# Kernel tuning notes

Hardware: AMD Instinct MI355X
Metric: run time of the kernel (lower is better)

The kernel has to match this reference:

```python
import jax, jax.numpy as jnp
import numpy as np

N_NODES = 50000
N_EDGES = 800000
F_NODE = 64
F_EDGE = 32
F_GLOBAL = 32
OUT_DIM = 64
N_GRAPHS = 256


def setup_inputs() -> dict:
    key = jax.random.key(0)
    ks = jax.random.split(key, 8)
    x = jax.random.normal(ks[0], (N_NODES, F_NODE), dtype=jnp.float32)
    edge_index = jax.random.randint(ks[1], (2, N_EDGES), 0, N_NODES, dtype=jnp.int64)
    edge_attr = jax.random.normal(ks[2], (N_EDGES, F_EDGE), dtype=jnp.float32)
    u = jax.random.normal(ks[3], (N_GRAPHS, F_GLOBAL), dtype=jnp.float32)
    batch = jnp.sort(jax.random.randint(ks[4], (N_NODES,), 0, N_GRAPHS, dtype=jnp.int64))
    # params (scaled like default Linear init)
    W1 = jax.random.normal(ks[5], (F_NODE + F_EDGE, OUT_DIM), dtype=jnp.float32) / np.sqrt(F_NODE + F_EDGE)
    b1 = jnp.zeros((OUT_DIM,), dtype=jnp.float32)
    W2 = jax.random.normal(ks[6], (F_NODE + OUT_DIM + F_GLOBAL, OUT_DIM), dtype=jnp.float32) / np.sqrt(F_NODE + OUT_DIM + F_GLOBAL)
    b2 = jnp.zeros((OUT_DIM,), dtype=jnp.float32)
    return {"x": x, "edge_index": edge_index, "edge_attr": edge_attr,
            "u": u, "batch": batch, "W1": W1, "b1": b1, "W2": W2, "b2": b2}


def reference(x, edge_index, edge_attr, u, batch, W1, b1, W2, b2):
    dest, src = edge_index[0], edge_index[1]
    # gather source node features + edge attrs -> [E, F_NODE + F_EDGE]
    edge_info = jnp.concatenate([x[src], edge_attr], axis=1)
    # node_mlp_1: Linear + ReLU
    edge_messages = jax.nn.relu(edge_info @ W1 + b1)  # [E, OUT_DIM]
    # scatter-sum into destination nodes
    aggregated = jax.ops.segment_sum(edge_messages, dest, num_segments=x.shape[0])  # [N, OUT_DIM]
    # concat node, aggregated messages, per-graph global
    node_info = jnp.concatenate([x, aggregated, u[batch]], axis=1)  # [N, F_NODE+OUT_DIM+F_GLOBAL]
    # node_mlp_2: Linear + ReLU
    return jax.nn.relu(node_info @ W2 + b2)  # [N, OUT_DIM]
```

## Files before the change

### kernel.cpp

```cpp
#include <hip/hip_runtime.h>
#include <hip/hip_bf16.h>

typedef __attribute__((ext_vector_type(8))) short short8;
typedef __attribute__((ext_vector_type(4))) float f32x4;

constexpr int NN = 50000;
constexpr int NE = 800000;
constexpr int FN = 64;
constexpr int FE = 32;
constexpr int FG = 32;
constexpr int OD = 64;
constexpr int NG = 256;

constexpr int SCAN_B = 256;
constexpr int NBLK = (NN + SCAN_B - 1) / SCAN_B;

constexpr int SLOTS_MAX = NE + 15 * NN;
constexpr int AGG_BLOCKS = 2048;
constexpr int AGG_WAVES  = AGG_BLOCKS * 4;
constexpr int NWIN       = NN / 16;
constexpr int NODE_BLOCKS = 512;
constexpr int NODE_WAVES  = NODE_BLOCKS * 4;

static __device__ __forceinline__ unsigned pack_bf16(float a, float b) {
    __hip_bfloat162 h = __float22bfloat162_rn(float2{a, b});
    return *reinterpret_cast<unsigned*>(&h);
}
static __device__ __forceinline__ float bf16r(float v) {
    __hip_bfloat16 h = __float2bfloat16(v);
    return __bfloat162float(h);
}

__global__ __launch_bounds__(256) void k_fill(int2* __restrict__ bucket,
                                              int* __restrict__ cnt,
                                              unsigned* __restrict__ xb32) {
    const int i = blockIdx.x * 256 + threadIdx.x;
    if (i < SLOTS_MAX) bucket[i] = make_int2(NN, 0);
    if (i < NN) cnt[i] = 0;
    if (i < 32) xb32[NN * 32 + i] = 0;
}

__global__ __launch_bounds__(256) void k_xcvt(const float* __restrict__ x,
                                              unsigned* __restrict__ xb32) {
    const int i = blockIdx.x * 256 + threadIdx.x;
    if (i >= NN * FN / 8) return;
    const float4* p = (const float4*)(x + (size_t)i * 8);
    float4 f0 = p[0], f1 = p[1];
    uint4 o;
    o.x = pack_bf16(f0.x, f0.y);
    o.y = pack_bf16(f0.z, f0.w);
    o.z = pack_bf16(f1.x, f1.y);
    o.w = pack_bf16(f1.z, f1.w);
    ((uint4*)xb32)[i] = o;
}

__global__ __launch_bounds__(256) void k_pre(const float* __restrict__ u,
                                             const float* __restrict__ W2,
                                             const float* __restrict__ b2,
                                             const float* __restrict__ ea,
                                             const float* __restrict__ W1,
                                             const float* __restrict__ b1,
                                             float* __restrict__ uW2b,
                                             float* __restrict__ corr) {
    if (blockIdx.x == NG / 4) {
        const int j = threadIdx.x;
        if (j < OD) {
            float acc = b1[j];
#pragma unroll
            for (int k = 0; k < FE; ++k) {
                const float ek = bf16r(ea[k]);
                const float wk = bf16r(W1[(FN + k) * OD + j]);
                acc = fmaf(ek, wk, acc);
            }
            corr[j] = fmaxf(acc, 0.0f);
        }
        return;
    }
    const int lane = threadIdx.x & 63;
    float wcol[FG];
#pragma unroll
    for (int k = 0; k < FG; ++k) wcol[k] = W2[(FN + OD + k) * OD + lane];
    const float bias = b2[lane];

    int g = (blockIdx.x * blockDim.x + threadIdx.x) >> 6;
    g = __builtin_amdgcn_readfirstlane(g);
    if (g >= NG) return;

    const float* __restrict__ urow = u + (size_t)g * FG;
    float acc = bias;
#pragma unroll
    for (int k = 0; k < FG; ++k) acc = fmaf(urow[k], wcol[k], acc);
    uW2b[(size_t)g * OD + lane] = acc;
}

__global__ __launch_bounds__(256) void k_hist(const int* __restrict__ ei,
                                              int* __restrict__ cnt) {
    const int e = blockIdx.x * blockDim.x + threadIdx.x;
    if (e < NE) atomicAdd(&cnt[ei[e]], 1);
}

__global__ __launch_bounds__(SCAN_B) void k_scan1(const int* __restrict__ cnt,
                                                  int* __restrict__ pstart,
                                                  int* __restrict__ bsum) {
    __shared__ int lds[SCAN_B];
    const int i = blockIdx.x * SCAN_B + threadIdx.x;
    const int v = (i < NN) ? (((cnt[i] + 15) >> 4) << 4) : 0;
    lds[threadIdx.x] = v;
    __syncthreads();
#pragma unroll
    for (int off = 1; off < SCAN_B; off <<= 1) {
        int t = (threadIdx.x >= off) ? lds[threadIdx.x - off] : 0;
        __syncthreads();
        lds[threadIdx.x] += t;
        __syncthreads();
    }
    const int incl = lds[threadIdx.x];
    if (i < NN) pstart[i] = incl - v;
    if (threadIdx.x == SCAN_B - 1) bsum[blockIdx.x] = incl;
}

__global__ __launch_bounds__(SCAN_B) void k_scan2(const int* __restrict__ bsum,
                                                  int* __restrict__ bscan) {
    __shared__ int lds[SCAN_B];
    const int i = threadIdx.x;
    const int v = (i < NBLK) ? bsum[i] : 0;
    lds[i] = v;
    __syncthreads();
#pragma unroll
    for (int off = 1; off < SCAN_B; off <<= 1) {
        int t = (i >= off) ? lds[i - off] : 0;
        __syncthreads();
        lds[i] += t;
        __syncthreads();
    }
    if (i < NBLK) bscan[i] = lds[i] - v;
}

__global__ __launch_bounds__(SCAN_B) void k_scan3(int* __restrict__ pstart,
                                                  const int* __restrict__ bscan,
                                                  const int* __restrict__ cnt,
                                                  int* __restrict__ cursor) {
    const int i = blockIdx.x * SCAN_B + threadIdx.x;
    if (i < NN) {
        const int s = pstart[i] + bscan[blockIdx.x];
        pstart[i] = s;
        cursor[i] = s;
        if (i == NN - 1) pstart[NN] = s + (((cnt[i] + 15) >> 4) << 4);
    }
}

__global__ __launch_bounds__(256) void k_scatter(const int* __restrict__ ei,
                                                 int* __restrict__ cursor,
                                                 int2* __restrict__ bucket) {
    const int e = blockIdx.x * blockDim.x + threadIdx.x;
    if (e < NE) {
        const int dst = ei[e];
        const int src = ei[NE + e];
        const int pos = atomicAdd(&cursor[dst], 1);
        bucket[pos] = make_int2(src, e);
    }
}

__global__ __launch_bounds__(256) void k_aggw(const int2* __restrict__ bucket,
                                              const float* __restrict__ ea,
                                              const unsigned short* __restrict__ xb,
                                              const float* __restrict__ W1,
                                              const float* __restrict__ b1,
                                              const int* __restrict__ pstart,
                                              float* __restrict__ partial) {
    const int l = threadIdx.x & 63;
    const int g = l >> 4;
    const int c = l & 15;

    short8 wf[3][4];
#pragma unroll
    for (int t = 0; t < 3; ++t)
#pragma unroll
        for (int b = 0; b < 4; ++b)
#pragma unroll
            for (int i = 0; i < 8; i += 2) {
                const int k = 32 * t + 8 * g + i;
                const unsigned p = pack_bf16(W1[k * OD + (c + 16 * b)],
                                             W1[(k + 1) * OD + (c + 16 * b)]);
                ((unsigned*)&wf[t][b])[i / 2] = p;
            }
    float bias[4];
#pragma unroll
    for (int b = 0; b < 4; ++b) bias[b] = b1[c + 16 * b];

    const int nwin = pstart[NN] >> 4;

    int wv = (blockIdx.x * blockDim.x + threadIdx.x) >> 6;
    wv = __builtin_amdgcn_readfirstlane(wv);

#pragma unroll 2
    for (int w = wv; w < nwin; w += AGG_WAVES) {
        const int2 se = bucket[(size_t)w * 16 + c];

        short8 a0, a1, a2;
        {
            const uint4* xr = (const uint4*)(xb + (size_t)se.x * FN);
            uint4 q0 = xr[g];
            uint4 q1 = xr[4 + g];
            a0 = *(short8*)&q0;
            a1 = *(short8*)&q1;
        }
        {
            const float4* er = (const float4*)(ea + (size_t)se.y * FE);
            float4 e0 = er[2 * g], e1 = er[2 * g + 1];
            uint4 q2;
            q2.x = pack_bf16(e0.x, e0.y);
            q2.y = pack_bf16(e0.z, e0.w);
            q2.z = pack_bf16(e1.x, e1.y);
            q2.w = pack_bf16(e1.z, e1.w);
            a2 = *(short8*)&q2;
        }

        float sv[4];
#pragma unroll
        for (int b = 0; b < 4; ++b) {
            f32x4 acc = {0.f, 0.f, 0.f, 0.f};
            acc = __builtin_amdgcn_mfma_f32_16x16x32_bf16(a0, wf[0][b], acc, 0, 0, 0);
            acc = __builtin_amdgcn_mfma_f32_16x16x32_bf16(a1, wf[1][b], acc, 0, 0, 0);
            acc = __builtin_amdgcn_mfma_f32_16x16x32_bf16(a2, wf[2][b], acc, 0, 0, 0);
            float s = fmaxf(acc[0] + bias[b], 0.0f) + fmaxf(acc[1] + bias[b], 0.0f)
                    + fmaxf(acc[2] + bias[b], 0.0f) + fmaxf(acc[3] + bias[b], 0.0f);
            s += __shfl_xor(s, 16);
            s += __shfl_xor(s, 32);
            sv[b] = s;
        }
        float v = sv[0];
        v = (g == 1) ? sv[1] : v;
        v = (g == 2) ? sv[2] : v;
        v = (g == 3) ? sv[3] : v;
        partial[(size_t)w * 64 + l] = v;
    }
}

__global__ __launch_bounds__(256) void k_red(const float* __restrict__ partial,
                                             const int* __restrict__ pstart,
                                             const int* __restrict__ cnt,
                                             const float* __restrict__ corr,
                                             unsigned short* __restrict__ aggb) {
    const int l = threadIdx.x & 63;
    int n = (blockIdx.x * blockDim.x + threadIdx.x) >> 6;
    n = __builtin_amdgcn_readfirstlane(n);
    if (n >= NN) return;

    const int w0 = pstart[n] >> 4;
    const int w1 = pstart[n + 1] >> 4;
    float s = 0.0f;
    for (int w = w0; w < w1; ++w) s += partial[(size_t)w * 64 + l];
    const int pads = ((w1 - w0) << 4) - cnt[n];
    s -= (float)pads * corr[l];
    __hip_bfloat16 hb = __float2bfloat16(s);
    aggb[(size_t)n * OD + l] = *reinterpret_cast<unsigned short*>(&hb);
}

__global__ __launch_bounds__(256) void k_nodem(const unsigned short* __restrict__ xb,
                                               const unsigned short* __restrict__ aggb,
                                               const int* __restrict__ bat,
                                               const float* __restrict__ uW2b,
                                               const float* __restrict__ W2,
                                               float* __restrict__ out) {
    const int l = threadIdx.x & 63;
    const int g = l >> 4;
    const int c = l & 15;

    short8 wf[4][4];
#pragma unroll
    for (int t = 0; t < 4; ++t)
#pragma unroll
        for (int b = 0; b < 4; ++b)
#pragma unroll
            for (int i = 0; i < 8; i += 2) {
                const int k = 32 * t + 8 * g + i;
                const unsigned p = pack_bf16(W2[k * OD + (c + 16 * b)],
                                             W2[(k + 1) * OD + (c + 16 * b)]);
                ((unsigned*)&wf[t][b])[i / 2] = p;
            }

    int wv = (blockIdx.x * blockDim.x + threadIdx.x) >> 6;
    wv = __builtin_amdgcn_readfirstlane(wv);

    for (int w = wv; w < NWIN; w += NODE_WAVES) {
        const int n0 = w * 16;
        const uint4* xr = (const uint4*)(xb + (size_t)(n0 + c) * FN);
        const uint4* ar = (const uint4*)(aggb + (size_t)(n0 + c) * OD);
        uint4 qx0 = xr[g], qx1 = xr[4 + g];
        uint4 qa0 = ar[g], qa1 = ar[4 + g];
        short8 a0 = *(short8*)&qx0, a1 = *(short8*)&qx1;
        short8 a2 = *(short8*)&qa0, a3 = *(short8*)&qa1;

        int bq[4];
#pragma unroll
        for (int q = 0; q < 4; ++q) bq[q] = bat[n0 + g * 4 + q];

#pragma unroll
        for (int b = 0; b < 4; ++b) {
            f32x4 acc = {0.f, 0.f, 0.f, 0.f};
            acc = __builtin_amdgcn_mfma_f32_16x16x32_bf16(a0, wf[0][b], acc, 0, 0, 0);
            acc = __builtin_amdgcn_mfma_f32_16x16x32_bf16(a1, wf[1][b], acc, 0, 0, 0);
            acc = __builtin_amdgcn_mfma_f32_16x16x32_bf16(a2, wf[2][b], acc, 0, 0, 0);
            acc = __builtin_amdgcn_mfma_f32_16x16x32_bf16(a3, wf[3][b], acc, 0, 0, 0);
#pragma unroll
            for (int q = 0; q < 4; ++q) {
                const int n = n0 + g * 4 + q;
                const float val = acc[q] + uW2b[(size_t)bq[q] * OD + c + 16 * b];
                out[(size_t)n * OD + c + 16 * b] = fmaxf(val, 0.0f);
            }
        }
    }
}

extern "C" void kernel_launch(void* const* d_in, const int* in_sizes, int n_in,
                              void* d_out, int out_size, void* d_ws, size_t ws_size,
                              hipStream_t stream) {
    const float* x    = (const float*)d_in[0];
    const int*   ei   = (const int*)d_in[1];
    const float* ea   = (const float*)d_in[2];
    const float* u    = (const float*)d_in[3];
    const int*   bat  = (const int*)d_in[4];
    const float* W1   = (const float*)d_in[5];
    const float* b1   = (const float*)d_in[6];
    const float* W2   = (const float*)d_in[7];
    const float* b2   = (const float*)d_in[8];
    float* out = (float*)d_out;

    char* ws = (char*)d_ws;
    auto alloc = [&](size_t bytes) {
        char* p = ws;
        ws += (bytes + 255) & ~size_t(255);
        return p;
    };
    unsigned short* xb   = (unsigned short*)alloc((size_t)(NN + 1) * FN * 2);
    unsigned short* aggb = (unsigned short*)alloc((size_t)NN * OD * 2);
    float* uW2b    = (float*)alloc((size_t)NG * OD * sizeof(float));
    float* corr    = (float*)alloc((size_t)OD * sizeof(float));
    int*   cnt     = (int*)alloc((size_t)NN * sizeof(int));
    int*   pstart  = (int*)alloc((size_t)(NN + 1) * sizeof(int));
    int*   cursor  = (int*)alloc((size_t)NN * sizeof(int));
    int*   bsum    = (int*)alloc((size_t)NBLK * sizeof(int));
    int*   bscan   = (int*)alloc((size_t)NBLK * sizeof(int));
    int2*  bucket  = (int2*)alloc((size_t)SLOTS_MAX * sizeof(int2));
    float* partial = (float*)alloc((size_t)(SLOTS_MAX / 16) * OD * sizeof(float));

    k_fill<<<dim3((SLOTS_MAX + 255) / 256), dim3(256), 0, stream>>>(bucket, cnt, (unsigned*)xb);

    k_xcvt<<<dim3((NN * FN / 8 + 255) / 256), dim3(256), 0, stream>>>(x, (unsigned*)xb);
    k_pre<<<dim3(NG / 4 + 1), dim3(256), 0, stream>>>(u, W2, b2, ea, W1, b1, uW2b, corr);

    k_hist<<<dim3((NE + 255) / 256), dim3(256), 0, stream>>>(ei, cnt);
    k_scan1<<<dim3(NBLK), dim3(SCAN_B), 0, stream>>>(cnt, pstart, bsum);
    k_scan2<<<dim3(1), dim3(SCAN_B), 0, stream>>>(bsum, bscan);
    k_scan3<<<dim3(NBLK), dim3(SCAN_B), 0, stream>>>(pstart, bscan, cnt, cursor);
    k_scatter<<<dim3((NE + 255) / 256), dim3(256), 0, stream>>>(ei, cursor, bucket);

    k_aggw<<<dim3(AGG_BLOCKS), dim3(256), 0, stream>>>(bucket, ea, xb, W1, b1, pstart, partial);
    k_red<<<dim3((NN * 64 + 255) / 256), dim3(256), 0, stream>>>(partial, pstart, cnt, corr, aggb);

    k_nodem<<<dim3(NODE_BLOCKS), dim3(256), 0, stream>>>(xb, aggb, bat, uW2b, W2, out);
}
```

Measured before the change: 173.5 us.

## Software-pipeline edge gathers in aggregation and replace full bucket fill with pad-only fill

The aggregation kernel now prefetches the next window's bucket entry and gathered node and edge features while computing the current window's MFMAs, hiding gather latency behind compute. The full-size bucket initialisation kernel is dropped: counts are cleared with a memset and only padding slots are written by a new per-node kernel after the scatter. Grid sizes for the aggregation and node kernels are retuned. This adds register pressure from the prefetch buffers and one extra small kernel launch.

```diff
diff --git a/kernel.cpp b/kernel.cpp
--- a/kernel.cpp
+++ b/kernel.cpp
@@ -16,10 +16,10 @@
 constexpr int NBLK = (NN + SCAN_B - 1) / SCAN_B;
 
 constexpr int SLOTS_MAX = NE + 15 * NN;
-constexpr int AGG_BLOCKS = 2048;
+constexpr int AGG_BLOCKS = 1280;
 constexpr int AGG_WAVES  = AGG_BLOCKS * 4;
 constexpr int NWIN       = NN / 16;
-constexpr int NODE_BLOCKS = 512;
+constexpr int NODE_BLOCKS = 782;
 constexpr int NODE_WAVES  = NODE_BLOCKS * 4;
 
 static __device__ __forceinline__ unsigned pack_bf16(float a, float b) {
@@ -31,18 +31,10 @@
     return __bfloat162float(h);
 }
 
-__global__ __launch_bounds__(256) void k_fill(int2* __restrict__ bucket,
-                                              int* __restrict__ cnt,
-                                              unsigned* __restrict__ xb32) {
-    const int i = blockIdx.x * 256 + threadIdx.x;
-    if (i < SLOTS_MAX) bucket[i] = make_int2(NN, 0);
-    if (i < NN) cnt[i] = 0;
-    if (i < 32) xb32[NN * 32 + i] = 0;
-}
-
 __global__ __launch_bounds__(256) void k_xcvt(const float* __restrict__ x,
                                               unsigned* __restrict__ xb32) {
     const int i = blockIdx.x * 256 + threadIdx.x;
+    if (i < 32 && blockIdx.x == 0) xb32[NN * 32 + i] = 0;
     if (i >= NN * FN / 8) return;
     const float4* p = (const float4*)(x + (size_t)i * 8);
     float4 f0 = p[0], f1 = p[1];
@@ -161,6 +153,18 @@
     }
 }
 
+__global__ __launch_bounds__(256) void k_padfill(const int* __restrict__ pstart,
+                                                 const int* __restrict__ cnt,
+                                                 int2* __restrict__ bucket) {
+    const int l = threadIdx.x & 63;
+    int n = (blockIdx.x * blockDim.x + threadIdx.x) >> 6;
+    n = __builtin_amdgcn_readfirstlane(n);
+    if (n >= NN) return;
+    const int base = pstart[n] + cnt[n];
+    const int pads = pstart[n + 1] - base;
+    if (l < pads) bucket[base + l] = make_int2(NN, 0);
+}
+
 __global__ __launch_bounds__(256) void k_aggw(const int2* __restrict__ bucket,
                                               const float* __restrict__ ea,
                                               const unsigned short* __restrict__ xb,
@@ -189,32 +193,46 @@
     for (int b = 0; b < 4; ++b) bias[b] = b1[c + 16 * b];
 
     const int nwin = pstart[NN] >> 4;
+    const int last = nwin - 1;
 
     int wv = (blockIdx.x * blockDim.x + threadIdx.x) >> 6;
     wv = __builtin_amdgcn_readfirstlane(wv);
-
-#pragma unroll 2
-    for (int w = wv; w < nwin; w += AGG_WAVES) {
+    if (wv >= nwin) return;
+
+    int w = wv;
+    uint4 q0, q1;
+    float4 e0, e1;
+    {
         const int2 se = bucket[(size_t)w * 16 + c];
-
-        short8 a0, a1, a2;
-        {
-            const uint4* xr = (const uint4*)(xb + (size_t)se.x * FN);
-            uint4 q0 = xr[g];
-            uint4 q1 = xr[4 + g];
-            a0 = *(short8*)&q0;
-            a1 = *(short8*)&q1;
-        }
-        {
-            const float4* er = (const float4*)(ea + (size_t)se.y * FE);
-            float4 e0 = er[2 * g], e1 = er[2 * g + 1];
-            uint4 q2;
-            q2.x = pack_bf16(e0.x, e0.y);
-            q2.y = pack_bf16(e0.z, e0.w);
-            q2.z = pack_bf16(e1.x, e1.y);
-            q2.w = pack_bf16(e1.z, e1.w);
-            a2 = *(short8*)&q2;
-        }
+        const uint4* xr = (const uint4*)(xb + (size_t)se.x * FN);
+        q0 = xr[g];
+        q1 = xr[4 + g];
+        const float4* er = (const float4*)(ea + (size_t)se.y * FE);
+        e0 = er[2 * g];
+        e1 = er[2 * g + 1];
+    }
+    int wn1 = w + AGG_WAVES;
+    int2 seB = bucket[(size_t)(wn1 > last ? last : wn1) * 16 + c];
+
+    while (w < nwin) {
+        int wn2 = w + 2 * AGG_WAVES;
+        const int2 seC = bucket[(size_t)(wn2 > last ? last : wn2) * 16 + c];
+
+        const uint4* xrn = (const uint4*)(xb + (size_t)seB.x * FN);
+        const uint4 q0n = xrn[g];
+        const uint4 q1n = xrn[4 + g];
+        const float4* ern = (const float4*)(ea + (size_t)seB.y * FE);
+        const float4 e0n = ern[2 * g];
+        const float4 e1n = ern[2 * g + 1];
+
+        short8 a0 = *(short8*)&q0;
+        short8 a1 = *(short8*)&q1;
+        uint4 q2;
+        q2.x = pack_bf16(e0.x, e0.y);
+        q2.y = pack_bf16(e0.z, e0.w);
+        q2.z = pack_bf16(e1.x, e1.y);
+        q2.w = pack_bf16(e1.z, e1.w);
+        short8 a2 = *(short8*)&q2;
 
         float sv[4];
 #pragma unroll
@@ -234,6 +252,11 @@
         v = (g == 2) ? sv[2] : v;
         v = (g == 3) ? sv[3] : v;
         partial[(size_t)w * 64 + l] = v;
+
+        q0 = q0n; q1 = q1n; e0 = e0n; e1 = e1n;
+        seB = seC;
+        w = wn1;
+        wn1 = w + AGG_WAVES;
     }
 }
 
@@ -345,7 +368,7 @@
     int2*  bucket  = (int2*)alloc((size_t)SLOTS_MAX * sizeof(int2));
     float* partial = (float*)alloc((size_t)(SLOTS_MAX / 16) * OD * sizeof(float));
 
-    k_fill<<<dim3((SLOTS_MAX + 255) / 256), dim3(256), 0, stream>>>(bucket, cnt, (unsigned*)xb);
+    hipMemsetAsync(cnt, 0, (size_t)NN * sizeof(int), stream);
 
     k_xcvt<<<dim3((NN * FN / 8 + 255) / 256), dim3(256), 0, stream>>>(x, (unsigned*)xb);
     k_pre<<<dim3(NG / 4 + 1), dim3(256), 0, stream>>>(u, W2, b2, ea, W1, b1, uW2b, corr);
@@ -355,6 +378,7 @@
     k_scan2<<<dim3(1), dim3(SCAN_B), 0, stream>>>(bsum, bscan);
     k_scan3<<<dim3(NBLK), dim3(SCAN_B), 0, stream>>>(pstart, bscan, cnt, cursor);
     k_scatter<<<dim3((NE + 255) / 256), dim3(256), 0, stream>>>(ei, cursor, bucket);
+    k_padfill<<<dim3((NN * 64 + 255) / 256), dim3(256), 0, stream>>>(pstart, cnt, bucket);
 
     k_aggw<<<dim3(AGG_BLOCKS), dim3(256), 0, stream>>>(bucket, ea, xb, W1, b1, pstart, partial);
     k_red<<<dim3((NN * 64 + 255) / 256), dim3(256), 0, stream>>>(partial, pstart, cnt, corr, aggb);
```

After: 181.6 us. 4.7% more time.

## Drop bucket prefill with per-window end masks and fuse setup kernels

Applied to the files above, without the earlier changes.

Removes the large bucket prefill kernel by recording, for each 16-slot window, the end index of its node's real edges. Padded slots are then clamped to a valid entry and masked in the ReLU sum, so the padding correction in the reduction is no longer needed. It also merges the x-to-bf16 conversion, count zeroing and global-feature precompute into one kernel, folds scan2 into scan3, and processes two windows per iteration so gather loads overlap. The node kernel block count also rises. In exchange it adds an extra winend write loop in the scan and extra compares in the aggregation kernel.

```diff
diff --git a/kernel.cpp b/kernel.cpp
--- a/kernel.cpp
+++ b/kernel.cpp
@@ -16,33 +16,47 @@
 constexpr int NBLK = (NN + SCAN_B - 1) / SCAN_B;
 
 constexpr int SLOTS_MAX = NE + 15 * NN;
+constexpr int NWIN_MAX  = SLOTS_MAX / 16;
+
+constexpr int XCVT_BLOCKS = (NN * FN / 8 + 255) / 256;
+constexpr int PRE_BLOCKS  = XCVT_BLOCKS + (NG * 64) / 256;
+
 constexpr int AGG_BLOCKS = 2048;
 constexpr int AGG_WAVES  = AGG_BLOCKS * 4;
-constexpr int NWIN       = NN / 16;
-constexpr int NODE_BLOCKS = 512;
+constexpr int NWIN_N = NN / 16;
+constexpr int NODE_BLOCKS = 782;
 constexpr int NODE_WAVES  = NODE_BLOCKS * 4;
 
 static __device__ __forceinline__ unsigned pack_bf16(float a, float b) {
     __hip_bfloat162 h = __float22bfloat162_rn(float2{a, b});
     return *reinterpret_cast<unsigned*>(&h);
 }
-static __device__ __forceinline__ float bf16r(float v) {
-    __hip_bfloat16 h = __float2bfloat16(v);
-    return __bfloat162float(h);
-}
-
-__global__ __launch_bounds__(256) void k_fill(int2* __restrict__ bucket,
-                                              int* __restrict__ cnt,
-                                              unsigned* __restrict__ xb32) {
+
+__global__ __launch_bounds__(256) void k_pre(const float* __restrict__ x,
+                                             unsigned* __restrict__ xb32,
+                                             const float* __restrict__ u,
+                                             const float* __restrict__ W2,
+                                             const float* __restrict__ b2,
+                                             float* __restrict__ uW2b,
+                                             int* __restrict__ cnt) {
+    if (blockIdx.x >= XCVT_BLOCKS) {
+        const int lane = threadIdx.x & 63;
+        float wcol[FG];
+#pragma unroll
+        for (int k = 0; k < FG; ++k) wcol[k] = W2[(FN + OD + k) * OD + lane];
+        const float bias = b2[lane];
+        int g = ((blockIdx.x - XCVT_BLOCKS) * 256 + threadIdx.x) >> 6;
+        g = __builtin_amdgcn_readfirstlane(g);
+        if (g >= NG) return;
+        const float* __restrict__ urow = u + (size_t)g * FG;
+        float acc = bias;
+#pragma unroll
+        for (int k = 0; k < FG; ++k) acc = fmaf(urow[k], wcol[k], acc);
+        uW2b[(size_t)g * OD + lane] = acc;
+        return;
+    }
     const int i = blockIdx.x * 256 + threadIdx.x;
-    if (i < SLOTS_MAX) bucket[i] = make_int2(NN, 0);
     if (i < NN) cnt[i] = 0;
-    if (i < 32) xb32[NN * 32 + i] = 0;
-}
-
-__global__ __launch_bounds__(256) void k_xcvt(const float* __restrict__ x,
-                                              unsigned* __restrict__ xb32) {
-    const int i = blockIdx.x * 256 + threadIdx.x;
     if (i >= NN * FN / 8) return;
     const float4* p = (const float4*)(x + (size_t)i * 8);
     float4 f0 = p[0], f1 = p[1];
@@ -54,45 +68,6 @@
     ((uint4*)xb32)[i] = o;
 }
 
-__global__ __launch_bounds__(256) void k_pre(const float* __restrict__ u,
-                                             const float* __restrict__ W2,
-                                             const float* __restrict__ b2,
-                                             const float* __restrict__ ea,
-                                             const float* __restrict__ W1,
-                                             const float* __restrict__ b1,
-                                             float* __restrict__ uW2b,
-                                             float* __restrict__ corr) {
-    if (blockIdx.x == NG / 4) {
-        const int j = threadIdx.x;
-        if (j < OD) {
-            float acc = b1[j];
-#pragma unroll
-            for (int k = 0; k < FE; ++k) {
-                const float ek = bf16r(ea[k]);
-                const float wk = bf16r(W1[(FN + k) * OD + j]);
-                acc = fmaf(ek, wk, acc);
-            }
-            corr[j] = fmaxf(acc, 0.0f);
-        }
-        return;
-    }
-    const int lane = threadIdx.x & 63;
-    float wcol[FG];
-#pragma unroll
-    for (int k = 0; k < FG; ++k) wcol[k] = W2[(FN + OD + k) * OD + lane];
-    const float bias = b2[lane];
-
-    int g = (blockIdx.x * blockDim.x + threadIdx.x) >> 6;
-    g = __builtin_amdgcn_readfirstlane(g);
-    if (g >= NG) return;
-
-    const float* __restrict__ urow = u + (size_t)g * FG;
-    float acc = bias;
-#pragma unroll
-    for (int k = 0; k < FG; ++k) acc = fmaf(urow[k], wcol[k], acc);
-    uW2b[(size_t)g * OD + lane] = acc;
-}
-
 __global__ __launch_bounds__(256) void k_hist(const int* __restrict__ ei,
                                               int* __restrict__ cnt) {
     const int e = blockIdx.x * blockDim.x + threadIdx.x;
@@ -119,33 +94,36 @@
     if (threadIdx.x == SCAN_B - 1) bsum[blockIdx.x] = incl;
 }
 
-__global__ __launch_bounds__(SCAN_B) void k_scan2(const int* __restrict__ bsum,
-                                                  int* __restrict__ bscan) {
+__global__ __launch_bounds__(SCAN_B) void k_scan23(int* __restrict__ pstart,
+                                                   const int* __restrict__ bsum,
+                                                   const int* __restrict__ cnt,
+                                                   int* __restrict__ cursor,
+                                                   int* __restrict__ winend) {
     __shared__ int lds[SCAN_B];
-    const int i = threadIdx.x;
-    const int v = (i < NBLK) ? bsum[i] : 0;
-    lds[i] = v;
+    const int t = threadIdx.x;
+    lds[t] = (t < NBLK) ? bsum[t] : 0;
     __syncthreads();
 #pragma unroll
     for (int off = 1; off < SCAN_B; off <<= 1) {
-        int t = (i >= off) ? lds[i - off] : 0;
+        int tv = (t >= off) ? lds[t - off] : 0;
         __syncthreads();
-        lds[i] += t;
+        lds[t] += tv;
         __syncthreads();
     }
-    if (i < NBLK) bscan[i] = lds[i] - v;
-}
-
-__global__ __launch_bounds__(SCAN_B) void k_scan3(int* __restrict__ pstart,
-                                                  const int* __restrict__ bscan,
-                                                  const int* __restrict__ cnt,
-                                                  int* __restrict__ cursor) {
-    const int i = blockIdx.x * SCAN_B + threadIdx.x;
+    const int boff = (blockIdx.x == 0) ? 0 : lds[blockIdx.x - 1];
+
+    const int i = blockIdx.x * SCAN_B + t;
     if (i < NN) {
-        const int s = pstart[i] + bscan[blockIdx.x];
+        const int cn = cnt[i];
+        const int pc = ((cn + 15) >> 4) << 4;
+        const int s = pstart[i] + boff;
         pstart[i] = s;
         cursor[i] = s;
-        if (i == NN - 1) pstart[NN] = s + (((cnt[i] + 15) >> 4) << 4);
+        const int end = s + cn;
+        const int w0 = s >> 4;
+        const int w1 = (s + pc) >> 4;
+        for (int w = w0; w < w1; ++w) winend[w] = end;
+        if (i == NN - 1) pstart[NN] = s + pc;
     }
 }
 
@@ -161,13 +139,14 @@
     }
 }
 
-__global__ __launch_bounds__(256) void k_aggw(const int2* __restrict__ bucket,
-                                              const float* __restrict__ ea,
-                                              const unsigned short* __restrict__ xb,
-                                              const float* __restrict__ W1,
-                                              const float* __restrict__ b1,
-                                              const int* __restrict__ pstart,
-                                              float* __restrict__ partial) {
+__global__ __launch_bounds__(256) void k_aggw2(const int2* __restrict__ bucket,
+                                               const float* __restrict__ ea,
+                                               const unsigned short* __restrict__ xb,
+                                               const float* __restrict__ W1,
+                                               const float* __restrict__ b1,
+                                               const int* __restrict__ pstart,
+                                               const int* __restrict__ winend,
+                                               float* __restrict__ partial) {
     const int l = threadIdx.x & 63;
     const int g = l >> 4;
     const int c = l & 15;
@@ -193,28 +172,16 @@
     int wv = (blockIdx.x * blockDim.x + threadIdx.x) >> 6;
     wv = __builtin_amdgcn_readfirstlane(wv);
 
-#pragma unroll 2
-    for (int w = wv; w < nwin; w += AGG_WAVES) {
-        const int2 se = bucket[(size_t)w * 16 + c];
-
-        short8 a0, a1, a2;
-        {
-            const uint4* xr = (const uint4*)(xb + (size_t)se.x * FN);
-            uint4 q0 = xr[g];
-            uint4 q1 = xr[4 + g];
-            a0 = *(short8*)&q0;
-            a1 = *(short8*)&q1;
-        }
-        {
-            const float4* er = (const float4*)(ea + (size_t)se.y * FE);
-            float4 e0 = er[2 * g], e1 = er[2 * g + 1];
-            uint4 q2;
-            q2.x = pack_bf16(e0.x, e0.y);
-            q2.y = pack_bf16(e0.z, e0.w);
-            q2.z = pack_bf16(e1.x, e1.y);
-            q2.w = pack_bf16(e1.z, e1.w);
-            a2 = *(short8*)&q2;
-        }
+    auto computeWin = [&](int w, int end, uint4 q0, uint4 q1,
+                          float4 e0, float4 e1) {
+        short8 a0 = *(short8*)&q0;
+        short8 a1 = *(short8*)&q1;
+        uint4 q2;
+        q2.x = pack_bf16(e0.x, e0.y);
+        q2.y = pack_bf16(e0.z, e0.w);
+        q2.z = pack_bf16(e1.x, e1.y);
+        q2.w = pack_bf16(e1.z, e1.w);
+        short8 a2 = *(short8*)&q2;
 
         float sv[4];
 #pragma unroll
@@ -223,8 +190,13 @@
             acc = __builtin_amdgcn_mfma_f32_16x16x32_bf16(a0, wf[0][b], acc, 0, 0, 0);
             acc = __builtin_amdgcn_mfma_f32_16x16x32_bf16(a1, wf[1][b], acc, 0, 0, 0);
             acc = __builtin_amdgcn_mfma_f32_16x16x32_bf16(a2, wf[2][b], acc, 0, 0, 0);
-            float s = fmaxf(acc[0] + bias[b], 0.0f) + fmaxf(acc[1] + bias[b], 0.0f)
-                    + fmaxf(acc[2] + bias[b], 0.0f) + fmaxf(acc[3] + bias[b], 0.0f);
+            float s = 0.0f;
+#pragma unroll
+            for (int q = 0; q < 4; ++q) {
+                const int row = w * 16 + 4 * g + q;
+                const float v = fmaxf(acc[q] + bias[b], 0.0f);
+                s += (row < end) ? v : 0.0f;
+            }
             s += __shfl_xor(s, 16);
             s += __shfl_xor(s, 32);
             sv[b] = s;
@@ -234,13 +206,45 @@
         v = (g == 2) ? sv[2] : v;
         v = (g == 3) ? sv[3] : v;
         partial[(size_t)w * 64 + l] = v;
+    };
+
+    for (int p = wv; 2 * p < nwin; p += AGG_WAVES) {
+        const int wA = 2 * p;
+        const int wB = wA + 1;
+        const bool hasB = (wB < nwin);
+
+        const int endA = winend[wA];
+        const int endB = winend[hasB ? wB : wA];
+
+        int sA = wA * 16 + c;
+        if (sA >= endA) sA = endA - 1;
+        int sB = wB * 16 + c;
+        if (!hasB || sB >= endB) sB = endB - 1;
+
+        const int2 pa = bucket[sA];
+        const int2 pb = bucket[sB];
+
+        const uint4* xra = (const uint4*)(xb + (size_t)pa.x * FN);
+        const uint4 qa0 = xra[g];
+        const uint4 qa1 = xra[4 + g];
+        const float4* era = (const float4*)(ea + (size_t)pa.y * FE);
+        const float4 ea0 = era[2 * g];
+        const float4 ea1 = era[2 * g + 1];
+
+        const uint4* xrb = (const uint4*)(xb + (size_t)pb.x * FN);
+        const uint4 qb0 = xrb[g];
+        const uint4 qb1 = xrb[4 + g];
+        const float4* erb = (const float4*)(ea + (size_t)pb.y * FE);
+        const float4 eb0 = erb[2 * g];
+        const float4 eb1 = erb[2 * g + 1];
+
+        computeWin(wA, endA, qa0, qa1, ea0, ea1);
+        if (hasB) computeWin(wB, endB, qb0, qb1, eb0, eb1);
     }
 }
 
 __global__ __launch_bounds__(256) void k_red(const float* __restrict__ partial,
                                              const int* __restrict__ pstart,
-                                             const int* __restrict__ cnt,
-                                             const float* __restrict__ corr,
                                              unsigned short* __restrict__ aggb) {
     const int l = threadIdx.x & 63;
     int n = (blockIdx.x * blockDim.x + threadIdx.x) >> 6;
@@ -251,8 +255,6 @@
     const int w1 = pstart[n + 1] >> 4;
     float s = 0.0f;
     for (int w = w0; w < w1; ++w) s += partial[(size_t)w * 64 + l];
-    const int pads = ((w1 - w0) << 4) - cnt[n];
-    s -= (float)pads * corr[l];
     __hip_bfloat16 hb = __float2bfloat16(s);
     aggb[(size_t)n * OD + l] = *reinterpret_cast<unsigned short*>(&hb);
 }
@@ -283,7 +285,7 @@
     int wv = (blockIdx.x * blockDim.x + threadIdx.x) >> 6;
     wv = __builtin_amdgcn_readfirstlane(wv);
 
-    for (int w = wv; w < NWIN; w += NODE_WAVES) {
+    for (int w = wv; w < NWIN_N; w += NODE_WAVES) {
         const int n0 = w * 16;
         const uint4* xr = (const uint4*)(xb + (size_t)(n0 + c) * FN);
         const uint4* ar = (const uint4*)(aggb + (size_t)(n0 + c) * OD);
@@ -333,31 +335,28 @@
         ws += (bytes + 255) & ~size_t(255);
         return p;
     };
-    unsigned short* xb   = (unsigned short*)alloc((size_t)(NN + 1) * FN * 2);
+    unsigned short* xb   = (unsigned short*)alloc((size_t)NN * FN * 2);
     unsigned short* aggb = (unsigned short*)alloc((size_t)NN * OD * 2);
     float* uW2b    = (float*)alloc((size_t)NG * OD * sizeof(float));
-    float* corr    = (float*)alloc((size_t)OD * sizeof(float));
     int*   cnt     = (int*)alloc((size_t)NN * sizeof(int));
     int*   pstart  = (int*)alloc((size_t)(NN + 1) * sizeof(int));
     int*   cursor  = (int*)alloc((size_t)NN * sizeof(int));
     int*   bsum    = (int*)alloc((size_t)NBLK * sizeof(int));
-    int*   bscan   = (int*)alloc((size_t)NBLK * sizeof(int));
+    int*   winend  = (int*)alloc((size_t)NWIN_MAX * sizeof(int));
     int2*  bucket  = (int2*)alloc((size_t)SLOTS_MAX * sizeof(int2));
-    float* partial = (float*)alloc((size_t)(SLOTS_MAX / 16) * OD * sizeof(float));
-
-    k_fill<<<dim3((SLOTS_MAX + 255) / 256), dim3(256), 0, stream>>>(bucket, cnt, (unsigned*)xb);
-
-    k_xcvt<<<dim3((NN * FN / 8 + 255) / 256), dim3(256), 0, stream>>>(x, (unsigned*)xb);
-    k_pre<<<dim3(NG / 4 + 1), dim3(256), 0, stream>>>(u, W2, b2, ea, W1, b1, uW2b, corr);
+    float* partial = (float*)alloc((size_t)NWIN_MAX * OD * sizeof(float));
+
+    k_pre<<<dim3(PRE_BLOCKS), dim3(256), 0, stream>>>(x, (unsigned*)xb, u, W2, b2, uW2b, cnt);
 
     k_hist<<<dim3((NE + 255) / 256), dim3(256), 0, stream>>>(ei, cnt);
     k_scan1<<<dim3(NBLK), dim3(SCAN_B), 0, stream>>>(cnt, pstart, bsum);
-    k_scan2<<<dim3(1), dim3(SCAN_B), 0, stream>>>(bsum, bscan);
-    k_scan3<<<dim3(NBLK), dim3(SCAN_B), 0, stream>>>(pstart, bscan, cnt, cursor);
+    k_scan23<<<dim3(NBLK), dim3(SCAN_B), 0, stream>>>(pstart, bsum, cnt, cursor, winend);
+
     k_scatter<<<dim3((NE + 255) / 256), dim3(256), 0, stream>>>(ei, cursor, bucket);
 
-    k_aggw<<<dim3(AGG_BLOCKS), dim3(256), 0, stream>>>(bucket, ea, xb, W1, b1, pstart, partial);
-    k_red<<<dim3((NN * 64 + 255) / 256), dim3(256), 0, stream>>>(partial, pstart, cnt, corr, aggb);
+    k_aggw2<<<dim3(AGG_BLOCKS), dim3(256), 0, stream>>>(bucket, ea, xb, W1, b1, pstart, winend, partial);
+
+    k_red<<<dim3((NN * 64 + 255) / 256), dim3(256), 0, stream>>>(partial, pstart, aggb);
 
     k_nodem<<<dim3(NODE_BLOCKS), dim3(256), 0, stream>>>(xb, aggb, bat, uW2b, W2, out);
 }
```

Result: faster. 168.8 us (-2.7%).
